# Performance work log

Hardware: AMD Instinct MI355X
Metric: run time of the kernel (lower is better)

The kernel has to match this reference:

```python
import jax, jax.numpy as jnp
import numpy as np
from jax import lax

PAD = 1  # 3x3 conv, stride 1, padding 1


def conv2d(x, w, b=None):
    # x: [B,C,H,W], w: [O,I,3,3]
    y = lax.conv_general_dilated(x, w, window_strides=(1, 1),
                                 padding=((PAD, PAD), (PAD, PAD)),
                                 dimension_numbers=("NCHW", "OIHW", "NCHW"))
    if b is not None:
        y = y + b[None, :, None, None]
    return y


def _bilinear(img, py, px):
    # img: [C,H,W]; py,px: [K,H,W] sampling coords (float). Zero padding outside.
    H, W = img.shape[1], img.shape[2]
    y0 = jnp.floor(py)
    x0 = jnp.floor(px)
    wy = py - y0  # [K,H,W]
    wx = px - x0
    y0i = y0.astype(jnp.int32)
    x0i = x0.astype(jnp.int32)

    def gather(yi, xi):
        valid = ((yi >= 0) & (yi < H) & (xi >= 0) & (xi < W)).astype(img.dtype)
        yc = jnp.clip(yi, 0, H - 1)
        xc = jnp.clip(xi, 0, W - 1)
        return img[:, yc, xc] * valid[None]  # [C,K,H,W]

    v00 = gather(y0i, x0i)
    v01 = gather(y0i, x0i + 1)
    v10 = gather(y0i + 1, x0i)
    v11 = gather(y0i + 1, x0i + 1)
    return (v00 * (1 - wy) * (1 - wx) + v01 * (1 - wy) * wx
            + v10 * wy * (1 - wx) + v11 * wy * wx)  # [C,K,H,W]


def reference(x, w_offset, b_offset, w_mask, b_mask, w_conv):
    B, C, H, W = x.shape
    K = 9  # 3x3 kernel taps
    offset = conv2d(x, w_offset, b_offset)              # [B,2K,H,W]
    mask = jax.nn.sigmoid(conv2d(x, w_mask, b_mask))    # [B,K,H,W]

    off = offset.reshape(B, K, 2, H, W)
    dy = off[:, :, 0]  # [B,K,H,W] (torchvision layout: y first)
    dx = off[:, :, 1]

    k = jnp.arange(K)
    ky = (k // 3).astype(x.dtype) - PAD  # tap row offset in {-1,0,1}
    kx = (k % 3).astype(x.dtype) - PAD
    ii = jnp.arange(H, dtype=x.dtype)
    jj = jnp.arange(W, dtype=x.dtype)

    py = ii[None, None, :, None] + ky[None, :, None, None] + dy  # [B,K,H,W]
    px = jj[None, None, None, :] + kx[None, :, None, None] + dx

    sampled = jax.vmap(_bilinear)(x, py, px)  # [B,C,K,H,W]
    sampled = sampled * mask[:, None]          # modulated deform-conv v2

    # weight [64,3,3,3] -> [O,C,K]; contract over C and kernel taps
    out = jnp.einsum('bckhw,ock->bohw', sampled, w_conv.reshape(w_conv.shape[0], C, K))
    return out


def setup_inputs() -> dict:
    key = jax.random.key(0)
    k = jax.random.split(key, 6)
    B, C, H, W = 16, 3, 256, 256
    return {
        'x': jax.random.normal(k[0], (B, C, H, W), jnp.float32),
        'w_offset': jax.random.normal(k[1], (18, 3, 3, 3), jnp.float32) * 0.1,
        'b_offset': jax.random.normal(k[2], (18,), jnp.float32) * 0.1,
        'w_mask': jax.random.normal(k[3], (9, 3, 3, 3), jnp.float32) * 0.1,
        'b_mask': jax.random.normal(k[4], (9,), jnp.float32) * 0.1,
        'w_conv': jax.random.normal(k[5], (64, 3, 3, 3), jnp.float32) * 0.1,
    }
```

## Files before the change

### kernel.cpp

```cpp
#include <hip/hip_runtime.h>
#include <hip/hip_bf16.h>

#define HH 256
#define WW 256
#define CC 3
#define KK 9
#define OC 64
#define KD 27
#define PSTS 40
#define MOFF 5120
#define MST 16
#define WRB 6144
#define XST (4 * WRB)
#define XSLOT 1024

typedef __attribute__((ext_vector_type(8))) short bf16x8;
typedef __attribute__((ext_vector_type(4))) short s16x4;
typedef __attribute__((ext_vector_type(4))) float f32x4;
typedef __attribute__((ext_vector_type(2))) float f32x2;
typedef __attribute__((ext_vector_type(2))) unsigned int u32x2;

static __device__ __forceinline__ short f2bf(float f) {
    __hip_bfloat16 h = __float2bfloat16(f);
    return __builtin_bit_cast(short, h);
}
static __device__ __forceinline__ unsigned pack2(short a, short b) {
    return (unsigned)(unsigned short)a | ((unsigned)(unsigned short)b << 16);
}
static __device__ __forceinline__ float bf2f(unsigned w) {
    return __uint_as_float(w << 16);
}
static __device__ __forceinline__ float bfup(unsigned w) {
    return __uint_as_float(w & 0xffff0000u);
}

__global__ __launch_bounds__(256) void dcn_prep(
    const float* __restrict__ x,
    const float* __restrict__ w_offset, const float* __restrict__ b_offset,
    const float* __restrict__ w_mask,   const float* __restrict__ b_mask,
    const float* __restrict__ w_conv,
    short* __restrict__ xbf, short* __restrict__ wcf, char* __restrict__ wof,
    int npix)
{
    const int tid = threadIdx.x;
    if (blockIdx.x == gridDim.x - 1) {
        if (tid < 64) {
            const int fm = tid & 15, kc = tid >> 4;
#pragma unroll
            for (int t = 0; t < 4; ++t) {
                bf16x8 v;
#pragma unroll
                for (int e = 0; e < 8; ++e) {
                    int kd = kc * 8 + e;
                    v[e] = (kd < KD) ? f2bf(w_conv[(t * 16 + fm) * KD + kd]) : (short)0;
                }
                *(bf16x8*)(wcf + tid * 32 + t * 8) = v;
            }
#pragma unroll
            for (int t = 0; t < 2; ++t) {
                int ch = t * 16 + fm;
                bf16x8 vh, vl;
#pragma unroll
                for (int e = 0; e < 8; ++e) {
                    int kd = kc * 8 + e;
                    float val = 0.0f;
                    if (kd < KD) {
                        if (ch < 18) val = w_offset[ch * KD + kd];
                        else if (ch < KD) val = w_mask[(ch - 18) * KD + kd];
                    }
                    unsigned u = __float_as_uint(val);
                    vh[e] = (short)(u >> 16);
                    float d = val - __uint_as_float(u & 0xffff0000u);
                    vl[e] = (short)(__float_as_uint(d) >> 16);
                }
                *(bf16x8*)(wof + tid * 96 + t * 16) = vh;
                *(bf16x8*)(wof + tid * 96 + 32 + t * 16) = vl;
            }
#pragma unroll
            for (int t = 0; t < 2; ++t) {
                f32x4 cb;
#pragma unroll
                for (int r = 0; r < 4; ++r) {
                    int ch = t * 16 + kc * 4 + r;
                    float v = 0.0f;
                    if (ch < 18) v = b_offset[ch];
                    else if (ch < KD) v = b_mask[ch - 18];
                    cb[r] = v;
                }
                *(f32x4*)(wof + tid * 96 + 64 + t * 16) = cb;
            }
        }
        return;
    }

    const int p0 = (blockIdx.x * 256 + tid) * 4;
    if (p0 >= npix) return;
    const int bb = p0 >> 16;
    const int q  = p0 & 0xffff;
    const float* xb = x + (size_t)bb * (3 * 65536) + q;
    f32x4 r0 = *(const f32x4*)(xb);
    f32x4 r1 = *(const f32x4*)(xb + 65536);
    f32x4 r2 = *(const f32x4*)(xb + 131072);

    bf16x8 v0 = {f2bf(r0[0]), f2bf(r1[0]), f2bf(r2[0]), 0,
                 f2bf(r0[1]), f2bf(r1[1]), f2bf(r2[1]), 0};
    bf16x8 v1 = {f2bf(r0[2]), f2bf(r1[2]), f2bf(r2[2]), 0,
                 f2bf(r0[3]), f2bf(r1[3]), f2bf(r2[3]), 0};
    short* A = xbf + (size_t)p0 * 4;
    *(bf16x8*)A       = v0;
    *(bf16x8*)(A + 8) = v1;
}

__global__ __launch_bounds__(256) void dcn_main(
    const float* __restrict__ x,
    const short* __restrict__ xbf,
    const short* __restrict__ wcf,
    const char*  __restrict__ wof,
    float* __restrict__ out)
{
    __shared__ __align__(16) char LDSBUF[XST + 7 * XSLOT * 2];

    const int tid = threadIdx.x;
    const int j = tid;
    const int i = blockIdx.x & (HH - 1);
    const int b = blockIdx.x >> 8;
    const int lane = tid & 63;
    const int wv = tid >> 6;
    const int fm = lane & 15;
    const int kc = lane >> 4;

    char* wbase = LDSBUF + wv * WRB;
    short* patchS = (short*)wbase;
    short* xs = (short*)(LDSBUF + XST);

    const float* xb = x + (size_t)b * (CC * HH * WW);
    const short* xrow = xbf + (size_t)b * (HH * WW * 4);

    u32x2 st[7];
#pragma unroll
    for (int s = 0; s < 7; ++s) {
        int gr = min(max(i - 3 + s, 0), HH - 1);
        st[s] = *(const u32x2*)(xrow + ((size_t)gr * WW + tid) * 4);
    }
#pragma unroll
    for (int s = 0; s < 7; ++s) {
        *(u32x2*)(xs + s * XSLOT + tid * 4) = st[s];
    }
    __syncthreads();

    const bool yok0 = (i - 1) >= 0, yok2 = (i + 1) < HH;
    const bool xok0 = (j - 1) >= 0, xok2 = (j + 1) < WW;
    s16x4 pr[3][3];
#pragma unroll
    for (int p = 0; p < 3; ++p) {
#pragma unroll
        for (int q = 0; q < 3; ++q) {
            int xx = min(max(j + q - 1, 0), WW - 1);
            pr[p][q] = *(const s16x4*)(xs + (p + 2) * XSLOT + xx * 4);
        }
    }
    {
        short* rp = patchS + lane * PSTS;
#pragma unroll
        for (int o = 0; o < 4; ++o) {
            bf16x8 vh;
#pragma unroll
            for (int e = 0; e < 8; ++e) {
                int kd = o * 8 + e;
                if (kd < KD) {
                    int c = kd / 9, rem = kd - c * 9, p = rem / 3, q = rem - p * 3;
                    bool ok = (p == 0 ? yok0 : (p == 2 ? yok2 : true)) &&
                              (q == 0 ? xok0 : (q == 2 ? xok2 : true));
                    vh[e] = ok ? pr[p][q][c] : (short)0;
                } else {
                    vh[e] = (short)0;
                }
            }
            *(bf16x8*)(rp + o * 8) = vh;
        }
    }

    const char* wl = wof + lane * 96;
    bf16x8 whi0 = *(const bf16x8*)(wl);
    bf16x8 whi1 = *(const bf16x8*)(wl + 16);
    bf16x8 wlo0 = *(const bf16x8*)(wl + 32);
    bf16x8 wlo1 = *(const bf16x8*)(wl + 48);
    f32x4 cb0 = *(const f32x4*)(wl + 64);
    f32x4 cb1 = *(const f32x4*)(wl + 80);

    f32x4 dacc[4][2];
#pragma unroll
    for (int g = 0; g < 4; ++g) {
        bf16x8 phi = *(const bf16x8*)(patchS + (g * 16 + fm) * PSTS + kc * 8);
        f32x4 a0 = __builtin_amdgcn_mfma_f32_16x16x32_bf16(whi0, phi, cb0, 0, 0, 0);
        a0 = __builtin_amdgcn_mfma_f32_16x16x32_bf16(wlo0, phi, a0, 0, 0, 0);
        f32x4 a1 = __builtin_amdgcn_mfma_f32_16x16x32_bf16(whi1, phi, cb1, 0, 0, 0);
        a1 = __builtin_amdgcn_mfma_f32_16x16x32_bf16(wlo1, phi, a1, 0, 0, 0);
        dacc[g][0] = a0;
        dacc[g][1] = a1;
    }
#pragma unroll
    for (int g = 0; g < 4; ++g) {
        int r = g * 16 + fm;
        char* dr = wbase + r * 80;
        char* mr = wbase + MOFF + r * MST;
        *(f32x4*)(dr + kc * 16) = dacc[g][0];
        f32x4 a1 = dacc[g][1];
        if (kc == 0) {
            *(f32x2*)(dr + 64) = (f32x2){a1[0], a1[1]};
            *(unsigned*)(dr + 72) = pack2(f2bf(a1[2]), f2bf(a1[3]));
        } else if (kc == 1) {
            *(unsigned*)(dr + 76) = pack2(f2bf(a1[0]), f2bf(a1[1]));
            *(unsigned*)(mr + 0) = pack2(f2bf(a1[2]), f2bf(a1[3]));
        } else if (kc == 2) {
            *(unsigned*)(mr + 4) = pack2(f2bf(a1[0]), f2bf(a1[1]));
            *(unsigned short*)(mr + 8) = (unsigned short)f2bf(a1[2]);
        }
    }

    const char* myD = wbase + lane * 80;
    f32x4 d03 = *(const f32x4*)(myD);
    f32x4 d47 = *(const f32x4*)(myD + 16);
    f32x4 d8b = *(const f32x4*)(myD + 32);
    f32x4 dcf = *(const f32x4*)(myD + 48);
    f32x2 d8p = *(const f32x2*)(myD + 64);
    u32x2 z03 = *(const u32x2*)(myD + 72);
    const char* myM = wbase + MOFF + lane * MST;
    u32x2 z47 = *(const u32x2*)(myM);
    unsigned z8w = *(const unsigned short*)(myM + 8);

    const float dyv[9] = {d03[0], d03[2], d47[0], d47[2], d8b[0], d8b[2], dcf[0], dcf[2], d8p[0]};
    const float dxv[9] = {d03[1], d03[3], d47[1], d47[3], d8b[1], d8b[3], dcf[1], dcf[3], d8p[1]};
    const float mzf[9] = {bf2f(z03.x), bfup(z03.x), bf2f(z03.y), bfup(z03.y),
                          bf2f(z47.x), bfup(z47.x), bf2f(z47.y), bfup(z47.y), bf2f(z8w)};

    bf16x8 afrag[4];
#pragma unroll
    for (int t2 = 0; t2 < 4; ++t2) afrag[t2] = *(const bf16x8*)(wcf + lane * 32 + t2 * 8);

    const float* x0p = xb;
    const float* x1p = xb + (size_t)HH * WW;
    const float* x2p = xb + (size_t)2 * HH * WW;
    float s27[KD];
#pragma unroll
    for (int k = 0; k < KK; ++k) {
        float dy = dyv[k], dx = dxv[k];
        float msk = 1.0f / (1.0f + __expf(-mzf[k]));

        float py = (float)(i + (k / 3) - 1) + dy;
        float px = (float)(j + (k % 3) - 1) + dx;
        float y0f = floorf(py), x0f = floorf(px);
        float wy = py - y0f, wx = px - x0f;
        int y0 = (int)y0f, x0 = (int)x0f;
        int y1 = y0 + 1, x1 = x0 + 1;

        float w00 = (1.0f - wy) * (1.0f - wx);
        float w01 = (1.0f - wy) * wx;
        float w10 = wy * (1.0f - wx);
        float w11 = wy * wx;

        bool v0y = (unsigned)y0 < HH, v1y = (unsigned)y1 < HH;
        bool v0x = (unsigned)x0 < WW, v1x = (unsigned)x1 < WW;
        float f00 = (v0y && v0x) ? w00 : 0.0f;
        float f01 = (v0y && v1x) ? w01 : 0.0f;
        float f10 = (v1y && v0x) ? w10 : 0.0f;
        float f11 = (v1y && v1x) ? w11 : 0.0f;

        int y0c = min(max(y0, 0), HH - 1), y1c = min(max(y1, 0), HH - 1);
        int s0 = y0c - i + 3;
        int s1 = y1c - i + 3;
        float r0, r1, r2;
        if (__builtin_expect(__any(((unsigned)s0 > 6u) || ((unsigned)s1 > 6u)), 0)) {
            int x0c = min(max(x0, 0), WW - 1), x1c = min(max(x1, 0), WW - 1);
            int o00 = y0c * WW + x0c, o01 = y0c * WW + x1c;
            int o10 = y1c * WW + x0c, o11 = y1c * WW + x1c;
            r0 = x0p[o00] * f00 + x0p[o01] * f01 + x0p[o10] * f10 + x0p[o11] * f11;
            r1 = x1p[o00] * f00 + x1p[o01] * f01 + x1p[o10] * f10 + x1p[o11] * f11;
            r2 = x2p[o00] * f00 + x2p[o01] * f01 + x2p[o10] * f10 + x2p[o11] * f11;
        } else {
            int xl = min(max(x0, 0), WW - 2);
            bool sw = (x0 != xl);
            const short* p0 = xs + s0 * XSLOT + xl * 4;
            const short* p1 = xs + s1 * XSLOT + xl * 4;
            u32x2 lo0 = *(const u32x2*)p0;
            u32x2 hi0 = *(const u32x2*)(p0 + 4);
            u32x2 lo1 = *(const u32x2*)p1;
            u32x2 hi1 = *(const u32x2*)(p1 + 4);

            float a0 = sw ? f01 : f00, b0 = sw ? f00 : f01;
            float a1w = sw ? f11 : f10, b1w = sw ? f10 : f11;

            r0 = fmaf(bf2f(lo0.x), a0, fmaf(bf2f(hi0.x), b0,
                 fmaf(bf2f(lo1.x), a1w, bf2f(hi1.x) * b1w)));
            r1 = fmaf(bfup(lo0.x), a0, fmaf(bfup(hi0.x), b0,
                 fmaf(bfup(lo1.x), a1w, bfup(hi1.x) * b1w)));
            r2 = fmaf(bf2f(lo0.y), a0, fmaf(bf2f(hi0.y), b0,
                 fmaf(bf2f(lo1.y), a1w, bf2f(hi1.y) * b1w)));
        }
        s27[k]      = r0 * msk;
        s27[9 + k]  = r1 * msk;
        s27[18 + k] = r2 * msk;
    }

    {
        short* srow = patchS + lane * PSTS;
#pragma unroll
        for (int o = 0; o < 4; ++o) {
            bf16x8 v;
#pragma unroll
            for (int e = 0; e < 8; ++e) {
                int kd = o * 8 + e;
                v[e] = (kd < KD) ? f2bf(s27[kd]) : (short)0;
            }
            *(bf16x8*)(srow + o * 8) = v;
        }
    }

    float* obase = out + ((size_t)b * OC * HH + i) * WW;
#pragma unroll
    for (int g = 0; g < 4; ++g) {
        bf16x8 sfrag = *(const bf16x8*)(patchS + (g * 16 + fm) * PSTS + kc * 8);
#pragma unroll
        for (int t2 = 0; t2 < 4; ++t2) {
            f32x4 acc = (f32x4){0.f, 0.f, 0.f, 0.f};
            acc = __builtin_amdgcn_mfma_f32_16x16x32_bf16(sfrag, afrag[t2], acc, 0, 0, 0);
            float* op = obase + (size_t)(t2 * 16 + fm) * (HH * WW) + (wv * 64 + g * 16 + kc * 4);
            *(f32x4*)op = acc;
        }
    }
}

extern "C" void kernel_launch(void* const* d_in, const int* in_sizes, int n_in,
                              void* d_out, int out_size, void* d_ws, size_t ws_size,
                              hipStream_t stream) {
    const float* x        = (const float*)d_in[0];
    const float* w_offset = (const float*)d_in[1];
    const float* b_offset = (const float*)d_in[2];
    const float* w_mask   = (const float*)d_in[3];
    const float* b_mask   = (const float*)d_in[4];
    const float* w_conv   = (const float*)d_in[5];
    float* out = (float*)d_out;

    int B = in_sizes[0] / (CC * HH * WW);
    int npix = B * HH * WW;

    short* xbf = (short*)d_ws;
    short* wcf = (short*)((char*)d_ws + (size_t)npix * 8);
    char*  wof = (char*)d_ws + (size_t)npix * 8 + 4096;

    int nb = (npix + 1023) / 1024;
    hipLaunchKernelGGL(dcn_prep, dim3(nb + 1), dim3(256), 0, stream,
                       x, w_offset, b_offset, w_mask, b_mask, w_conv,
                       xbf, wcf, wof, npix);
    hipLaunchKernelGGL(dcn_main, dim3(B * HH), dim3(256), 0, stream,
                       x, xbf, wcf, wof, out);
}
```

Baseline: 75.84 us.

## Process four output rows per block sharing a ten-row LDS input window

Each block now handles four consecutive image rows instead of one, loading a ten-row bf16 input window into shared memory once and looping over the rows. This cuts redundant halo row loads (7 rows per output row before) and amortizes the weight/fragment loads and block launch overhead. It reduces the grid to a quarter as many blocks and serializes rows within a block, which lowers parallelism and latency hiding. Per-wave LDS scratch is reused across iterations without a barrier, which works only because each wave touches its own region.

```diff
diff --git a/kernel.cpp b/kernel.cpp
--- a/kernel.cpp
+++ b/kernel.cpp
@@ -13,6 +13,8 @@
 #define WRB 6144
 #define XST (4 * WRB)
 #define XSLOT 1024
+#define ROWS 4
+#define SLOTS 10
 
 typedef __attribute__((ext_vector_type(8))) short bf16x8;
 typedef __attribute__((ext_vector_type(4))) short s16x4;
@@ -118,12 +120,12 @@
     const char*  __restrict__ wof,
     float* __restrict__ out)
 {
-    __shared__ __align__(16) char LDSBUF[XST + 7 * XSLOT * 2];
+    __shared__ __align__(16) char LDSBUF[XST + SLOTS * XSLOT * 2];
 
     const int tid = threadIdx.x;
     const int j = tid;
-    const int i = blockIdx.x & (HH - 1);
-    const int b = blockIdx.x >> 8;
+    const int r0 = (blockIdx.x & 63) * ROWS;
+    const int b = blockIdx.x >> 6;
     const int lane = tid & 63;
     const int wv = tid >> 6;
     const int fm = lane & 15;
@@ -136,49 +138,19 @@
     const float* xb = x + (size_t)b * (CC * HH * WW);
     const short* xrow = xbf + (size_t)b * (HH * WW * 4);
 
-    u32x2 st[7];
-#pragma unroll
-    for (int s = 0; s < 7; ++s) {
-        int gr = min(max(i - 3 + s, 0), HH - 1);
-        st[s] = *(const u32x2*)(xrow + ((size_t)gr * WW + tid) * 4);
-    }
-#pragma unroll
-    for (int s = 0; s < 7; ++s) {
-        *(u32x2*)(xs + s * XSLOT + tid * 4) = st[s];
+    {
+        u32x2 st[SLOTS];
+#pragma unroll
+        for (int s = 0; s < SLOTS; ++s) {
+            int gr = min(max(r0 - 3 + s, 0), HH - 1);
+            st[s] = *(const u32x2*)(xrow + ((size_t)gr * WW + tid) * 4);
+        }
+#pragma unroll
+        for (int s = 0; s < SLOTS; ++s) {
+            *(u32x2*)(xs + s * XSLOT + tid * 4) = st[s];
+        }
     }
     __syncthreads();
-
-    const bool yok0 = (i - 1) >= 0, yok2 = (i + 1) < HH;
-    const bool xok0 = (j - 1) >= 0, xok2 = (j + 1) < WW;
-    s16x4 pr[3][3];
-#pragma unroll
-    for (int p = 0; p < 3; ++p) {
-#pragma unroll
-        for (int q = 0; q < 3; ++q) {
-            int xx = min(max(j + q - 1, 0), WW - 1);
-            pr[p][q] = *(const s16x4*)(xs + (p + 2) * XSLOT + xx * 4);
-        }
-    }
-    {
-        short* rp = patchS + lane * PSTS;
-#pragma unroll
-        for (int o = 0; o < 4; ++o) {
-            bf16x8 vh;
-#pragma unroll
-            for (int e = 0; e < 8; ++e) {
-                int kd = o * 8 + e;
-                if (kd < KD) {
-                    int c = kd / 9, rem = kd - c * 9, p = rem / 3, q = rem - p * 3;
-                    bool ok = (p == 0 ? yok0 : (p == 2 ? yok2 : true)) &&
-                              (q == 0 ? xok0 : (q == 2 ? xok2 : true));
-                    vh[e] = ok ? pr[p][q][c] : (short)0;
-                } else {
-                    vh[e] = (short)0;
-                }
-            }
-            *(bf16x8*)(rp + o * 8) = vh;
-        }
-    }
 
     const char* wl = wof + lane * 96;
     bf16x8 whi0 = *(const bf16x8*)(wl);
@@ -187,53 +159,6 @@
     bf16x8 wlo1 = *(const bf16x8*)(wl + 48);
     f32x4 cb0 = *(const f32x4*)(wl + 64);
     f32x4 cb1 = *(const f32x4*)(wl + 80);
-
-    f32x4 dacc[4][2];
-#pragma unroll
-    for (int g = 0; g < 4; ++g) {
-        bf16x8 phi = *(const bf16x8*)(patchS + (g * 16 + fm) * PSTS + kc * 8);
-        f32x4 a0 = __builtin_amdgcn_mfma_f32_16x16x32_bf16(whi0, phi, cb0, 0, 0, 0);
-        a0 = __builtin_amdgcn_mfma_f32_16x16x32_bf16(wlo0, phi, a0, 0, 0, 0);
-        f32x4 a1 = __builtin_amdgcn_mfma_f32_16x16x32_bf16(whi1, phi, cb1, 0, 0, 0);
-        a1 = __builtin_amdgcn_mfma_f32_16x16x32_bf16(wlo1, phi, a1, 0, 0, 0);
-        dacc[g][0] = a0;
-        dacc[g][1] = a1;
-    }
-#pragma unroll
-    for (int g = 0; g < 4; ++g) {
-        int r = g * 16 + fm;
-        char* dr = wbase + r * 80;
-        char* mr = wbase + MOFF + r * MST;
-        *(f32x4*)(dr + kc * 16) = dacc[g][0];
-        f32x4 a1 = dacc[g][1];
-        if (kc == 0) {
-            *(f32x2*)(dr + 64) = (f32x2){a1[0], a1[1]};
-            *(unsigned*)(dr + 72) = pack2(f2bf(a1[2]), f2bf(a1[3]));
-        } else if (kc == 1) {
-            *(unsigned*)(dr + 76) = pack2(f2bf(a1[0]), f2bf(a1[1]));
-            *(unsigned*)(mr + 0) = pack2(f2bf(a1[2]), f2bf(a1[3]));
-        } else if (kc == 2) {
-            *(unsigned*)(mr + 4) = pack2(f2bf(a1[0]), f2bf(a1[1]));
-            *(unsigned short*)(mr + 8) = (unsigned short)f2bf(a1[2]);
-        }
-    }
-
-    const char* myD = wbase + lane * 80;
-    f32x4 d03 = *(const f32x4*)(myD);
-    f32x4 d47 = *(const f32x4*)(myD + 16);
-    f32x4 d8b = *(const f32x4*)(myD + 32);
-    f32x4 dcf = *(const f32x4*)(myD + 48);
-    f32x2 d8p = *(const f32x2*)(myD + 64);
-    u32x2 z03 = *(const u32x2*)(myD + 72);
-    const char* myM = wbase + MOFF + lane * MST;
-    u32x2 z47 = *(const u32x2*)(myM);
-    unsigned z8w = *(const unsigned short*)(myM + 8);
-
-    const float dyv[9] = {d03[0], d03[2], d47[0], d47[2], d8b[0], d8b[2], dcf[0], dcf[2], d8p[0]};
-    const float dxv[9] = {d03[1], d03[3], d47[1], d47[3], d8b[1], d8b[3], dcf[1], dcf[3], d8p[1]};
-    const float mzf[9] = {bf2f(z03.x), bfup(z03.x), bf2f(z03.y), bfup(z03.y),
-                          bf2f(z47.x), bfup(z47.x), bf2f(z47.y), bfup(z47.y), bf2f(z8w)};
-
     bf16x8 afrag[4];
 #pragma unroll
     for (int t2 = 0; t2 < 4; ++t2) afrag[t2] = *(const bf16x8*)(wcf + lane * 32 + t2 * 8);
@@ -241,91 +166,176 @@
     const float* x0p = xb;
     const float* x1p = xb + (size_t)HH * WW;
     const float* x2p = xb + (size_t)2 * HH * WW;
-    float s27[KD];
-#pragma unroll
-    for (int k = 0; k < KK; ++k) {
-        float dy = dyv[k], dx = dxv[k];
-        float msk = 1.0f / (1.0f + __expf(-mzf[k]));
-
-        float py = (float)(i + (k / 3) - 1) + dy;
-        float px = (float)(j + (k % 3) - 1) + dx;
-        float y0f = floorf(py), x0f = floorf(px);
-        float wy = py - y0f, wx = px - x0f;
-        int y0 = (int)y0f, x0 = (int)x0f;
-        int y1 = y0 + 1, x1 = x0 + 1;
-
-        float w00 = (1.0f - wy) * (1.0f - wx);
-        float w01 = (1.0f - wy) * wx;
-        float w10 = wy * (1.0f - wx);
-        float w11 = wy * wx;
-
-        bool v0y = (unsigned)y0 < HH, v1y = (unsigned)y1 < HH;
-        bool v0x = (unsigned)x0 < WW, v1x = (unsigned)x1 < WW;
-        float f00 = (v0y && v0x) ? w00 : 0.0f;
-        float f01 = (v0y && v1x) ? w01 : 0.0f;
-        float f10 = (v1y && v0x) ? w10 : 0.0f;
-        float f11 = (v1y && v1x) ? w11 : 0.0f;
-
-        int y0c = min(max(y0, 0), HH - 1), y1c = min(max(y1, 0), HH - 1);
-        int s0 = y0c - i + 3;
-        int s1 = y1c - i + 3;
-        float r0, r1, r2;
-        if (__builtin_expect(__any(((unsigned)s0 > 6u) || ((unsigned)s1 > 6u)), 0)) {
-            int x0c = min(max(x0, 0), WW - 1), x1c = min(max(x1, 0), WW - 1);
-            int o00 = y0c * WW + x0c, o01 = y0c * WW + x1c;
-            int o10 = y1c * WW + x0c, o11 = y1c * WW + x1c;
-            r0 = x0p[o00] * f00 + x0p[o01] * f01 + x0p[o10] * f10 + x0p[o11] * f11;
-            r1 = x1p[o00] * f00 + x1p[o01] * f01 + x1p[o10] * f10 + x1p[o11] * f11;
-            r2 = x2p[o00] * f00 + x2p[o01] * f01 + x2p[o10] * f10 + x2p[o11] * f11;
-        } else {
-            int xl = min(max(x0, 0), WW - 2);
-            bool sw = (x0 != xl);
-            const short* p0 = xs + s0 * XSLOT + xl * 4;
-            const short* p1 = xs + s1 * XSLOT + xl * 4;
-            u32x2 lo0 = *(const u32x2*)p0;
-            u32x2 hi0 = *(const u32x2*)(p0 + 4);
-            u32x2 lo1 = *(const u32x2*)p1;
-            u32x2 hi1 = *(const u32x2*)(p1 + 4);
-
-            float a0 = sw ? f01 : f00, b0 = sw ? f00 : f01;
-            float a1w = sw ? f11 : f10, b1w = sw ? f10 : f11;
-
-            r0 = fmaf(bf2f(lo0.x), a0, fmaf(bf2f(hi0.x), b0,
-                 fmaf(bf2f(lo1.x), a1w, bf2f(hi1.x) * b1w)));
-            r1 = fmaf(bfup(lo0.x), a0, fmaf(bfup(hi0.x), b0,
-                 fmaf(bfup(lo1.x), a1w, bfup(hi1.x) * b1w)));
-            r2 = fmaf(bf2f(lo0.y), a0, fmaf(bf2f(hi0.y), b0,
-                 fmaf(bf2f(lo1.y), a1w, bf2f(hi1.y) * b1w)));
-        }
-        s27[k]      = r0 * msk;
-        s27[9 + k]  = r1 * msk;
-        s27[18 + k] = r2 * msk;
-    }
-
-    {
-        short* srow = patchS + lane * PSTS;
-#pragma unroll
-        for (int o = 0; o < 4; ++o) {
-            bf16x8 v;
-#pragma unroll
-            for (int e = 0; e < 8; ++e) {
-                int kd = o * 8 + e;
-                v[e] = (kd < KD) ? f2bf(s27[kd]) : (short)0;
-            }
-            *(bf16x8*)(srow + o * 8) = v;
-        }
-    }
-
-    float* obase = out + ((size_t)b * OC * HH + i) * WW;
-#pragma unroll
-    for (int g = 0; g < 4; ++g) {
-        bf16x8 sfrag = *(const bf16x8*)(patchS + (g * 16 + fm) * PSTS + kc * 8);
-#pragma unroll
-        for (int t2 = 0; t2 < 4; ++t2) {
-            f32x4 acc = (f32x4){0.f, 0.f, 0.f, 0.f};
-            acc = __builtin_amdgcn_mfma_f32_16x16x32_bf16(sfrag, afrag[t2], acc, 0, 0, 0);
-            float* op = obase + (size_t)(t2 * 16 + fm) * (HH * WW) + (wv * 64 + g * 16 + kc * 4);
-            *(f32x4*)op = acc;
+
+#pragma unroll 1
+    for (int d = 0; d < ROWS; ++d) {
+        const int ri = r0 + d;
+
+        const bool yok0 = (ri - 1) >= 0, yok2 = (ri + 1) < HH;
+        const bool xok0 = (j - 1) >= 0, xok2 = (j + 1) < WW;
+        s16x4 pr[3][3];
+#pragma unroll
+        for (int p = 0; p < 3; ++p) {
+#pragma unroll
+            for (int q = 0; q < 3; ++q) {
+                int xx = min(max(j + q - 1, 0), WW - 1);
+                pr[p][q] = *(const s16x4*)(xs + (d + p + 2) * XSLOT + xx * 4);
+            }
+        }
+        {
+            short* rp = patchS + lane * PSTS;
+#pragma unroll
+            for (int o = 0; o < 4; ++o) {
+                bf16x8 vh;
+#pragma unroll
+                for (int e = 0; e < 8; ++e) {
+                    int kd = o * 8 + e;
+                    if (kd < KD) {
+                        int c = kd / 9, rem = kd - c * 9, p = rem / 3, q = rem - p * 3;
+                        bool ok = (p == 0 ? yok0 : (p == 2 ? yok2 : true)) &&
+                                  (q == 0 ? xok0 : (q == 2 ? xok2 : true));
+                        vh[e] = ok ? pr[p][q][c] : (short)0;
+                    } else {
+                        vh[e] = (short)0;
+                    }
+                }
+                *(bf16x8*)(rp + o * 8) = vh;
+            }
+        }
+
+        f32x4 dacc[4][2];
+#pragma unroll
+        for (int g = 0; g < 4; ++g) {
+            bf16x8 phi = *(const bf16x8*)(patchS + (g * 16 + fm) * PSTS + kc * 8);
+            f32x4 a0 = __builtin_amdgcn_mfma_f32_16x16x32_bf16(whi0, phi, cb0, 0, 0, 0);
+            a0 = __builtin_amdgcn_mfma_f32_16x16x32_bf16(wlo0, phi, a0, 0, 0, 0);
+            f32x4 a1 = __builtin_amdgcn_mfma_f32_16x16x32_bf16(whi1, phi, cb1, 0, 0, 0);
+            a1 = __builtin_amdgcn_mfma_f32_16x16x32_bf16(wlo1, phi, a1, 0, 0, 0);
+            dacc[g][0] = a0;
+            dacc[g][1] = a1;
+        }
+#pragma unroll
+        for (int g = 0; g < 4; ++g) {
+            int r = g * 16 + fm;
+            char* dr = wbase + r * 80;
+            char* mr = wbase + MOFF + r * MST;
+            *(f32x4*)(dr + kc * 16) = dacc[g][0];
+            f32x4 a1 = dacc[g][1];
+            if (kc == 0) {
+                *(f32x2*)(dr + 64) = (f32x2){a1[0], a1[1]};
+                *(unsigned*)(dr + 72) = pack2(f2bf(a1[2]), f2bf(a1[3]));
+            } else if (kc == 1) {
+                *(unsigned*)(dr + 76) = pack2(f2bf(a1[0]), f2bf(a1[1]));
+                *(unsigned*)(mr + 0) = pack2(f2bf(a1[2]), f2bf(a1[3]));
+            } else if (kc == 2) {
+                *(unsigned*)(mr + 4) = pack2(f2bf(a1[0]), f2bf(a1[1]));
+                *(unsigned short*)(mr + 8) = (unsigned short)f2bf(a1[2]);
+            }
+        }
+
+        const char* myD = wbase + lane * 80;
+        f32x4 d03 = *(const f32x4*)(myD);
+        f32x4 d47 = *(const f32x4*)(myD + 16);
+        f32x4 d8b = *(const f32x4*)(myD + 32);
+        f32x4 dcf = *(const f32x4*)(myD + 48);
+        f32x2 d8p = *(const f32x2*)(myD + 64);
+        u32x2 z03 = *(const u32x2*)(myD + 72);
+        const char* myM = wbase + MOFF + lane * MST;
+        u32x2 z47 = *(const u32x2*)(myM);
+        unsigned z8w = *(const unsigned short*)(myM + 8);
+
+        const float dyv[9] = {d03[0], d03[2], d47[0], d47[2], d8b[0], d8b[2], dcf[0], dcf[2], d8p[0]};
+        const float dxv[9] = {d03[1], d03[3], d47[1], d47[3], d8b[1], d8b[3], dcf[1], dcf[3], d8p[1]};
+        const float mzf[9] = {bf2f(z03.x), bfup(z03.x), bf2f(z03.y), bfup(z03.y),
+                              bf2f(z47.x), bfup(z47.x), bf2f(z47.y), bfup(z47.y), bf2f(z8w)};
+
+        float s27[KD];
+#pragma unroll
+        for (int k = 0; k < KK; ++k) {
+            float dy = dyv[k], dx = dxv[k];
+            float msk = 1.0f / (1.0f + __expf(-mzf[k]));
+
+            float py = (float)(ri + (k / 3) - 1) + dy;
+            float px = (float)(j + (k % 3) - 1) + dx;
+            float y0f = floorf(py), x0f = floorf(px);
+            float wy = py - y0f, wx = px - x0f;
+            int y0 = (int)y0f, x0 = (int)x0f;
+            int y1 = y0 + 1, x1 = x0 + 1;
+
+            float w00 = (1.0f - wy) * (1.0f - wx);
+            float w01 = (1.0f - wy) * wx;
+            float w10 = wy * (1.0f - wx);
+            float w11 = wy * wx;
+
+            bool v0y = (unsigned)y0 < HH, v1y = (unsigned)y1 < HH;
+            bool v0x = (unsigned)x0 < WW, v1x = (unsigned)x1 < WW;
+            float f00 = (v0y && v0x) ? w00 : 0.0f;
+            float f01 = (v0y && v1x) ? w01 : 0.0f;
+            float f10 = (v1y && v0x) ? w10 : 0.0f;
+            float f11 = (v1y && v1x) ? w11 : 0.0f;
+
+            int y0c = min(max(y0, 0), HH - 1), y1c = min(max(y1, 0), HH - 1);
+            int s0 = y0c - r0 + 3;
+            int s1 = y1c - r0 + 3;
+            float r0v_, r1v_, r2v_;
+            if (__builtin_expect(__any(((unsigned)s0 > (SLOTS - 1)) ||
+                                       ((unsigned)s1 > (SLOTS - 1))), 0)) {
+                int x0c = min(max(x0, 0), WW - 1), x1c = min(max(x1, 0), WW - 1);
+                int o00 = y0c * WW + x0c, o01 = y0c * WW + x1c;
+                int o10 = y1c * WW + x0c, o11 = y1c * WW + x1c;
+                r0v_ = x0p[o00] * f00 + x0p[o01] * f01 + x0p[o10] * f10 + x0p[o11] * f11;
+                r1v_ = x1p[o00] * f00 + x1p[o01] * f01 + x1p[o10] * f10 + x1p[o11] * f11;
+                r2v_ = x2p[o00] * f00 + x2p[o01] * f01 + x2p[o10] * f10 + x2p[o11] * f11;
+            } else {
+                int xl = min(max(x0, 0), WW - 2);
+                bool sw = (x0 != xl);
+                const short* p0 = xs + s0 * XSLOT + xl * 4;
+                const short* p1 = xs + s1 * XSLOT + xl * 4;
+                u32x2 lo0 = *(const u32x2*)p0;
+                u32x2 hi0 = *(const u32x2*)(p0 + 4);
+                u32x2 lo1 = *(const u32x2*)p1;
+                u32x2 hi1 = *(const u32x2*)(p1 + 4);
+
+                float a0 = sw ? f01 : f00, b0 = sw ? f00 : f01;
+                float a1w = sw ? f11 : f10, b1w = sw ? f10 : f11;
+
+                r0v_ = fmaf(bf2f(lo0.x), a0, fmaf(bf2f(hi0.x), b0,
+                       fmaf(bf2f(lo1.x), a1w, bf2f(hi1.x) * b1w)));
+                r1v_ = fmaf(bfup(lo0.x), a0, fmaf(bfup(hi0.x), b0,
+                       fmaf(bfup(lo1.x), a1w, bfup(hi1.x) * b1w)));
+                r2v_ = fmaf(bf2f(lo0.y), a0, fmaf(bf2f(hi0.y), b0,
+                       fmaf(bf2f(lo1.y), a1w, bf2f(hi1.y) * b1w)));
+            }
+            s27[k]      = r0v_ * msk;
+            s27[9 + k]  = r1v_ * msk;
+            s27[18 + k] = r2v_ * msk;
+        }
+
+        {
+            short* srow = patchS + lane * PSTS;
+#pragma unroll
+            for (int o = 0; o < 4; ++o) {
+                bf16x8 v;
+#pragma unroll
+                for (int e = 0; e < 8; ++e) {
+                    int kd = o * 8 + e;
+                    v[e] = (kd < KD) ? f2bf(s27[kd]) : (short)0;
+                }
+                *(bf16x8*)(srow + o * 8) = v;
+            }
+        }
+
+        float* obase = out + ((size_t)b * OC * HH + ri) * WW;
+#pragma unroll
+        for (int g = 0; g < 4; ++g) {
+            bf16x8 sfrag = *(const bf16x8*)(patchS + (g * 16 + fm) * PSTS + kc * 8);
+#pragma unroll
+            for (int t2 = 0; t2 < 4; ++t2) {
+                f32x4 acc = (f32x4){0.f, 0.f, 0.f, 0.f};
+                acc = __builtin_amdgcn_mfma_f32_16x16x32_bf16(sfrag, afrag[t2], acc, 0, 0, 0);
+                float* op = obase + (size_t)(t2 * 16 + fm) * (HH * WW) + (wv * 64 + g * 16 + kc * 4);
+                *(f32x4*)op = acc;
+            }
         }
     }
 }
@@ -352,6 +362,6 @@
     hipLaunchKernelGGL(dcn_prep, dim3(nb + 1), dim3(256), 0, stream,
                        x, w_offset, b_offset, w_mask, b_mask, w_conv,
                        xbf, wcf, wof, npix);
-    hipLaunchKernelGGL(dcn_main, dim3(B * HH), dim3(256), 0, stream,
+    hipLaunchKernelGGL(dcn_main, dim3(B * (HH / ROWS)), dim3(256), 0, stream,
                        x, xbf, wcf, wof, out);
 }
```

After: 75.74 us. No clear change (-0.1%).
